# Kernel optimization log

Measured on AMD Instinct MI355X. Metric: run time of the kernel, lower is better.

The kernel has to match this reference:

```python
import jax, jax.numpy as jnp
import numpy as np

DN = ('NCHW', 'OIHW', 'NCHW')

def _conv(x, w, b, pad):
    y = jax.lax.conv_general_dilated(x, w, (1, 1), pad, dimension_numbers=DN)
    return y + b[None, :, None, None]

def setup_inputs() -> dict:
    key = jax.random.key(0)
    ks = jax.random.split(key, 8)
    B, C, H, W = 8, 256, 64, 64
    C8 = C // 8
    return {
        'x': jax.random.normal(ks[0], (B, C, H, W), jnp.float32),
        'wq': jax.random.normal(ks[1], (C8, C, 1, 3), jnp.float32) * 0.02,
        'bq': jax.random.normal(ks[2], (C8,), jnp.float32) * 0.02,
        'wk': jax.random.normal(ks[3], (C8, C, 3, 1), jnp.float32) * 0.02,
        'bk': jax.random.normal(ks[4], (C8,), jnp.float32) * 0.02,
        'wv': jax.random.normal(ks[5], (C, C, 1, 1), jnp.float32) * 0.02,
        'bv': jax.random.normal(ks[6], (C,), jnp.float32) * 0.02,
        'gamma': jax.random.normal(ks[7], (1,), jnp.float32),
    }

def reference(x, wq, bq, wk, bk, wv, bv, gamma):
    B, C, H, W = x.shape
    N = H * W
    # q: (1,3) kernel, pad (0,1); k: (3,1) kernel, pad (1,0); v: 1x1
    q = _conv(x, wq, bq, [(0, 0), (1, 1)]).reshape(B, -1, N)  # B, C/8, N
    k = _conv(x, wk, bk, [(1, 1), (0, 0)]).reshape(B, -1, N)  # B, C/8, N
    v = _conv(x, wv, bv, [(0, 0), (0, 0)]).reshape(B, C, N)   # B, C, N
    affinity = jnp.einsum('bci,bcj->bij', q, k)               # B, N, N
    affinity = jax.nn.softmax(affinity, axis=-1)
    # weights = v @ affinity^T  ->  (B, C, N)
    weights = jnp.einsum('bcj,bij->bci', v, affinity).reshape(B, C, H, W)
    return gamma[0] * weights + x
```

## Files before the change

### kernel.cpp

```cpp
#include <hip/hip_runtime.h>
#include <math.h>

#define BB 8
#define CCH 256
#define C8 32
#define NN 4096
#define LOG2E 1.44269504f

typedef unsigned short us;
typedef __attribute__((ext_vector_type(8))) short bf16x8;
typedef __attribute__((ext_vector_type(4))) float f32x4;
typedef __attribute__((ext_vector_type(16))) float f32x16;

static __device__ __forceinline__ us f2bf(float f) {
  union { float f; unsigned u; } v; v.f = f;
  unsigned r = v.u + 0x7fffu + ((v.u >> 16) & 1u);
  return (us)(r >> 16);
}
static __device__ __forceinline__ us f2bf_rhu(float f) {
  return (us)((__float_as_uint(f) + 0x8000u) >> 16);
}
template <int CTRL>
static __device__ __forceinline__ float dpp_mv(float x) {
  return __int_as_float(
      __builtin_amdgcn_update_dpp(0, __float_as_int(x), CTRL, 0xF, 0xF, false));
}
static __device__ __forceinline__ float rowsum16(float t) {
  t += dpp_mv<0x121>(t);
  t += dpp_mv<0x122>(t);
  t += dpp_mv<0x124>(t);
  t += dpp_mv<0x128>(t);
  return t;
}

__global__ __launch_bounds__(256) void prep_kernel(
    const float* __restrict__ x, const float* __restrict__ wq,
    const float* __restrict__ wk, const float* __restrict__ wv,
    us* __restrict__ xT, us* __restrict__ wqc, us* __restrict__ wkc,
    us* __restrict__ wvb) {
  __shared__ __align__(16) us lt[64 * 68];
  int bid = blockIdx.x;
  int tid = threadIdx.x;
  if (bid < 2048) {
    int b = bid >> 8, cb = (bid >> 6) & 3, nb = bid & 63;
    const float* xb = x + (((size_t)(b * 256 + cb * 64)) << 12);
    int nl = tid & 63, ch = tid >> 6;
#pragma unroll
    for (int p = 0; p < 16; p++) {
      int c = p * 4 + ch;
      lt[nl * 68 + c] = f2bf(xb[((size_t)c << 12) + (nb * 64 + nl)]);
    }
    __syncthreads();
    us* xTb = xT + (((size_t)b << 12) + nb * 64) * 256 + cb * 64;
    int cw = tid & 7, nr0 = tid >> 3;
#pragma unroll
    for (int p2 = 0; p2 < 2; p2++) {
      int nr = p2 * 32 + nr0;
      uint2 lo = *(const uint2*)&lt[nr * 68 + cw * 8];
      uint2 hi = *(const uint2*)&lt[nr * 68 + cw * 8 + 4];
      *(uint4*)&xTb[(size_t)nr * 256 + cw * 8] = make_uint4(lo.x, lo.y, hi.x, hi.y);
    }
  } else {
    int idx = (bid - 2048) * 256 + tid;
    if (idx < 24576) {
      int oc = idx / 768, r = idx % 768, t = r >> 8, ic = r & 255;
      wqc[idx] = f2bf(wq[(oc * 256 + ic) * 3 + t] * LOG2E);
    } else if (idx < 49152) {
      int j = idx - 24576;
      int oc = j / 768, r = j % 768, t = r >> 8, ic = r & 255;
      wkc[j] = f2bf(wk[(oc * 256 + ic) * 3 + t]);
    } else if (idx < 114688) {
      int j = idx - 49152;
      wvb[j] = f2bf(wv[j]);
    }
  }
}

__global__ __launch_bounds__(256) void conv_kernel(
    const us* __restrict__ xT, const us* __restrict__ wqc,
    const us* __restrict__ wkc, const float* __restrict__ bq,
    const float* __restrict__ bk, const us* __restrict__ wvb,
    const float* __restrict__ bv, us* __restrict__ qT, us* __restrict__ kT,
    us* __restrict__ vblk) {
  int tid = threadIdx.x, lane = tid & 63, w = tid >> 6;
  int l15 = lane & 15, quad = lane >> 4;
  if (blockIdx.x < 512) {
    int bid = blockIdx.x;
    int b = bid & 7, rt = bid >> 3;
    int n0 = rt * 64, y = rt;
    bool isq = (w < 2);
    int m0 = (w & 1) * 16;
    const us* wc = isq ? wqc : wkc;
    const us* xTb = xT + (((size_t)b << 12) * 256);
    f32x4 acc[4];
#pragma unroll
    for (int nt = 0; nt < 4; nt++) acc[nt] = (f32x4){0.f, 0.f, 0.f, 0.f};
#pragma unroll
    for (int t = 0; t < 3; t++) {
      bool killT = (!isq) && ((t == 0 && y == 0) || (t == 2 && y == 63));
      if (!killT) {
        int dn = isq ? (t - 1) : (t - 1) * 64;
#pragma unroll
        for (int k8 = 0; k8 < 8; k8++) {
          int kloc = t * 256 + k8 * 32 + quad * 8;
          bf16x8 af = *(const bf16x8*)(wc + (size_t)(m0 + l15) * 768 + kloc);
          int ic = k8 * 32 + quad * 8;
#pragma unroll
          for (int nt = 0; nt < 4; nt++) {
            int nl = nt * 16 + l15;
            int ns = n0 + nl + dn;
            ns = ns < 0 ? 0 : (ns > 4095 ? 4095 : ns);
            bf16x8 bf = *(const bf16x8*)(xTb + (size_t)ns * 256 + ic);
            if (isq && ((t == 0 && nl == 0) || (t == 2 && nl == 63)))
              bf = (bf16x8){0, 0, 0, 0, 0, 0, 0, 0};
            acc[nt] = __builtin_amdgcn_mfma_f32_16x16x32_bf16(af, bf, acc[nt], 0, 0, 0);
          }
        }
      }
    }
    const float* bias = isq ? bq : bk;
    float bsc = isq ? LOG2E : 1.0f;
    us* outp = (isq ? qT : kT) + (((size_t)b << 12) * 32);
    float b0 = bias[m0 + quad * 4 + 0] * bsc;
    float b1 = bias[m0 + quad * 4 + 1] * bsc;
    float b2 = bias[m0 + quad * 4 + 2] * bsc;
    float b3 = bias[m0 + quad * 4 + 3] * bsc;
#pragma unroll
    for (int nt = 0; nt < 4; nt++) {
      int n = n0 + nt * 16 + l15;
      unsigned lo = (unsigned)f2bf(acc[nt][0] + b0) | ((unsigned)f2bf(acc[nt][1] + b1) << 16);
      unsigned hi = (unsigned)f2bf(acc[nt][2] + b2) | ((unsigned)f2bf(acc[nt][3] + b3) << 16);
      *(uint2*)(outp + (size_t)n * 32 + m0 + quad * 4) = make_uint2(lo, hi);
    }
  } else {
    int bid = blockIdx.x - 512;
    int b = bid & 7, nt0 = bid >> 3;
    int n0 = nt0 * 64;
    const us* xTb = xT + (((size_t)b << 12) * 256);
    f32x4 acc[4][4];
#pragma unroll
    for (int ct = 0; ct < 4; ct++)
#pragma unroll
      for (int nt = 0; nt < 4; nt++) acc[ct][nt] = (f32x4){0.f, 0.f, 0.f, 0.f};
#pragma unroll
    for (int kk = 0; kk < 8; kk++) {
      bf16x8 bfr[4];
#pragma unroll
      for (int nt = 0; nt < 4; nt++)
        bfr[nt] = *(const bf16x8*)(xTb + (size_t)(n0 + nt * 16 + l15) * 256 + kk * 32 + quad * 8);
#pragma unroll
      for (int ct = 0; ct < 4; ct++) {
        bf16x8 af = *(const bf16x8*)(wvb + (size_t)(w * 64 + ct * 16 + l15) * 256 + kk * 32 + quad * 8);
#pragma unroll
        for (int nt = 0; nt < 4; nt++)
          acc[ct][nt] = __builtin_amdgcn_mfma_f32_16x16x32_bf16(af, bfr[nt], acc[ct][nt], 0, 0, 0);
      }
    }
    us* vb = vblk + ((size_t)b << 20);
#pragma unroll
    for (int ct = 0; ct < 4; ct++) {
#pragma unroll
      for (int r = 0; r < 4; r++) {
        int oc = w * 64 + ct * 16 + quad * 4 + r;
        float bvv = bv[oc];
#pragma unroll
        for (int nt = 0; nt < 4; nt++) {
          vb[((size_t)((n0 >> 4) + nt) * 256 + oc) * 16 + l15] = f2bf(acc[ct][nt][r] + bvv);
        }
      }
    }
  }
}

__global__ __launch_bounds__(512, 4) void attn_kernel(
    const float* __restrict__ x, const us* __restrict__ qT,
    const us* __restrict__ kT, const us* __restrict__ vblk,
    const float* __restrict__ gamma_p, float* __restrict__ out) {
  __shared__ __align__(16) us pb[2][64 * 72];
  __shared__ float lpart[2][64];

  int tid = threadIdx.x, lane = tid & 63, w = tid >> 6;
  int l15 = lane & 15, quad = lane >> 4;
  int l31 = lane & 31, h32 = lane >> 5;
  int tw = w & 3, jh = w >> 2;

  int bid = blockIdx.x;
  int b = bid & 7, i0 = (bid >> 3) * 64;

  const us* qTb = qT + (((size_t)b << 12) * 32);
  const us* kTb = kT + (((size_t)b << 12) * 32);
  const us* vbb = vblk + ((size_t)b << 20);

  bf16x8 qf = *(const bf16x8*)(qTb + (size_t)(i0 + tw * 16 + l15) * 32 + quad * 8);

  float lr[4] = {0.f, 0.f, 0.f, 0.f};
  f32x16 o[2];
#pragma unroll
  for (int it = 0; it < 2; it++)
#pragma unroll
    for (int rg = 0; rg < 16; rg++) o[it][rg] = 0.f;

  int bu = 0;
  for (int jt = 0; jt < 64; jt++) {
    int j0 = jt * 64;
    bf16x8 kf0 = *(const bf16x8*)(kTb + (size_t)(j0 + jh * 32 + l15) * 32 + quad * 8);
    bf16x8 kf1 = *(const bf16x8*)(kTb + (size_t)(j0 + jh * 32 + 16 + l15) * 32 + quad * 8);
    bf16x8 vf[4];
#pragma unroll
    for (int ks = 0; ks < 4; ks++)
      vf[ks] = *(const bf16x8*)(vbb + ((size_t)((j0 >> 4) + ks) * 256 + w * 32 + l31) * 16 + h32 * 8);
    f32x4 s0 = __builtin_amdgcn_mfma_f32_16x16x32_bf16(qf, kf0, (f32x4){0.f, 0.f, 0.f, 0.f}, 0, 0, 0);
    f32x4 s1 = __builtin_amdgcn_mfma_f32_16x16x32_bf16(qf, kf1, (f32x4){0.f, 0.f, 0.f, 0.f}, 0, 0, 0);
    us* pw = &pb[bu][(tw * 16 + quad * 4) * 72 + jh * 32 + l15];
#pragma unroll
    for (int r = 0; r < 4; r++) {
      float p0 = __builtin_amdgcn_exp2f(s0[r]);
      float p1 = __builtin_amdgcn_exp2f(s1[r]);
      lr[r] += p0 + p1;
      pw[r * 72] = f2bf_rhu(p0);
      pw[r * 72 + 16] = f2bf_rhu(p1);
    }
    __syncthreads();
#pragma unroll
    for (int ks = 0; ks < 4; ks++) {
      bf16x8 pf0 = *(const bf16x8*)&pb[bu][(size_t)l31 * 72 + ks * 16 + h32 * 8];
      bf16x8 pf1 = *(const bf16x8*)&pb[bu][(size_t)(32 + l31) * 72 + ks * 16 + h32 * 8];
      o[0] = __builtin_amdgcn_mfma_f32_32x32x16_bf16(vf[ks], pf0, o[0], 0, 0, 0);
      o[1] = __builtin_amdgcn_mfma_f32_32x32x16_bf16(vf[ks], pf1, o[1], 0, 0, 0);
    }
    bu ^= 1;
  }

  float ls[4];
#pragma unroll
  for (int r = 0; r < 4; r++) ls[r] = rowsum16(lr[r]);
  if (l15 == 0) {
#pragma unroll
    for (int r = 0; r < 4; r++) lpart[jh][tw * 16 + quad * 4 + r] = ls[r];
  }
  __syncthreads();
  float g = gamma_p[0];
  const float* xb = x + ((size_t)b << 20);
  float* ob = out + ((size_t)b << 20);
  float gl[2];
#pragma unroll
  for (int it = 0; it < 2; it++) {
    int i = it * 32 + l31;
    gl[it] = g / (lpart[0][i] + lpart[1][i]);
  }
#pragma unroll
  for (int it = 0; it < 2; it++) {
    int i = i0 + it * 32 + l31;
#pragma unroll
    for (int rg = 0; rg < 16; rg++) {
      int c = w * 32 + ((rg & 3) + 8 * (rg >> 2) + 4 * h32);
      size_t idx = ((size_t)c << 12) + i;
      ob[idx] = o[it][rg] * gl[it] + xb[idx];
    }
  }
}

extern "C" void kernel_launch(void* const* d_in, const int* in_sizes, int n_in,
                              void* d_out, int out_size, void* d_ws, size_t ws_size,
                              hipStream_t stream) {
  const float* x = (const float*)d_in[0];
  const float* wq = (const float*)d_in[1];
  const float* bq = (const float*)d_in[2];
  const float* wk = (const float*)d_in[3];
  const float* bk = (const float*)d_in[4];
  const float* wv = (const float*)d_in[5];
  const float* bv = (const float*)d_in[6];
  const float* gamma = (const float*)d_in[7];
  float* out = (float*)d_out;

  us* xT = (us*)d_ws;
  us* qT = xT + (size_t)8388608;
  us* kT = qT + (size_t)1048576;
  us* vblk = kT + (size_t)1048576;
  us* wqc = vblk + (size_t)8388608;
  us* wkc = wqc + (size_t)24576;
  us* wvb = wkc + (size_t)24576;

  prep_kernel<<<2496, 256, 0, stream>>>(x, wq, wk, wv, xT, wqc, wkc, wvb);
  conv_kernel<<<1024, 256, 0, stream>>>(xT, wqc, wkc, bq, bk, wvb, bv, qT, kT, vblk);
  attn_kernel<<<512, 512, 0, stream>>>(x, qT, kT, vblk, gamma, out);
}
```

Before: 234.0 us.

## Software-pipeline K/V loads, transpose score MFMA, pack bf16 conversions in attention loop

Restructures the attention main loop to prefetch the next tile's K and V fragments into alternate register sets, with a two-step unrolled macro. The score MFMA operands are swapped (K×Q) so each lane holds four consecutive j values, enabling packed v_cvt_pk_bf16_f32 conversions and 64-bit LDS stores of P. It adds s_setprio around the MFMA sections and an explicit lgkmcnt wait plus barrier. The row-sum reduction changes to two cross-lane shuffles. This is meant to hide global load latency and cut per-element conversion and LDS store cost, at the price of more VGPRs, which could reduce occupancy.

```diff
diff --git a/kernel.cpp b/kernel.cpp
--- a/kernel.cpp
+++ b/kernel.cpp
@@ -16,21 +16,6 @@
   union { float f; unsigned u; } v; v.f = f;
   unsigned r = v.u + 0x7fffu + ((v.u >> 16) & 1u);
   return (us)(r >> 16);
-}
-static __device__ __forceinline__ us f2bf_rhu(float f) {
-  return (us)((__float_as_uint(f) + 0x8000u) >> 16);
-}
-template <int CTRL>
-static __device__ __forceinline__ float dpp_mv(float x) {
-  return __int_as_float(
-      __builtin_amdgcn_update_dpp(0, __float_as_int(x), CTRL, 0xF, 0xF, false));
-}
-static __device__ __forceinline__ float rowsum16(float t) {
-  t += dpp_mv<0x121>(t);
-  t += dpp_mv<0x122>(t);
-  t += dpp_mv<0x124>(t);
-  t += dpp_mv<0x128>(t);
-  return t;
 }
 
 __global__ __launch_bounds__(256) void prep_kernel(
@@ -193,51 +178,100 @@
 
   bf16x8 qf = *(const bf16x8*)(qTb + (size_t)(i0 + tw * 16 + l15) * 32 + quad * 8);
 
-  float lr[4] = {0.f, 0.f, 0.f, 0.f};
-  f32x16 o[2];
-#pragma unroll
-  for (int it = 0; it < 2; it++)
-#pragma unroll
-    for (int rg = 0; rg < 16; rg++) o[it][rg] = 0.f;
-
-  int bu = 0;
-  for (int jt = 0; jt < 64; jt++) {
-    int j0 = jt * 64;
-    bf16x8 kf0 = *(const bf16x8*)(kTb + (size_t)(j0 + jh * 32 + l15) * 32 + quad * 8);
-    bf16x8 kf1 = *(const bf16x8*)(kTb + (size_t)(j0 + jh * 32 + 16 + l15) * 32 + quad * 8);
-    bf16x8 vf[4];
-#pragma unroll
-    for (int ks = 0; ks < 4; ks++)
-      vf[ks] = *(const bf16x8*)(vbb + ((size_t)((j0 >> 4) + ks) * 256 + w * 32 + l31) * 16 + h32 * 8);
-    f32x4 s0 = __builtin_amdgcn_mfma_f32_16x16x32_bf16(qf, kf0, (f32x4){0.f, 0.f, 0.f, 0.f}, 0, 0, 0);
-    f32x4 s1 = __builtin_amdgcn_mfma_f32_16x16x32_bf16(qf, kf1, (f32x4){0.f, 0.f, 0.f, 0.f}, 0, 0, 0);
-    us* pw = &pb[bu][(tw * 16 + quad * 4) * 72 + jh * 32 + l15];
-#pragma unroll
-    for (int r = 0; r < 4; r++) {
-      float p0 = __builtin_amdgcn_exp2f(s0[r]);
-      float p1 = __builtin_amdgcn_exp2f(s1[r]);
-      lr[r] += p0 + p1;
-      pw[r * 72] = f2bf_rhu(p0);
-      pw[r * 72 + 16] = f2bf_rhu(p1);
-    }
-    __syncthreads();
-#pragma unroll
-    for (int ks = 0; ks < 4; ks++) {
-      bf16x8 pf0 = *(const bf16x8*)&pb[bu][(size_t)l31 * 72 + ks * 16 + h32 * 8];
-      bf16x8 pf1 = *(const bf16x8*)&pb[bu][(size_t)(32 + l31) * 72 + ks * 16 + h32 * 8];
-      o[0] = __builtin_amdgcn_mfma_f32_32x32x16_bf16(vf[ks], pf0, o[0], 0, 0, 0);
-      o[1] = __builtin_amdgcn_mfma_f32_32x32x16_bf16(vf[ks], pf1, o[1], 0, 0, 0);
-    }
-    bu ^= 1;
-  }
-
-  float ls[4];
-#pragma unroll
-  for (int r = 0; r < 4; r++) ls[r] = rowsum16(lr[r]);
-  if (l15 == 0) {
-#pragma unroll
-    for (int r = 0; r < 4; r++) lpart[jh][tw * 16 + quad * 4 + r] = ls[r];
-  }
+  const us* kbase = kTb + (size_t)(jh * 32 + l15) * 32 + quad * 8;
+  const us* vbase = vbb + (size_t)(w * 32 + l31) * 16 + h32 * 8;
+  int pwi = (tw * 16 + l15) * 72 + jh * 32 + quad * 4;
+  int pri = l31 * 72 + h32 * 8;
+
+  float lr = 0.f;
+  f32x16 o0, o1;
+#pragma unroll
+  for (int rg = 0; rg < 16; rg++) { o0[rg] = 0.f; o1[rg] = 0.f; }
+
+  bf16x8 kA0, kA1, vA0, vA1, vA2, vA3;
+  bf16x8 kB0, kB1, vB0, vB1, vB2, vB3;
+  kA0 = *(const bf16x8*)(kbase);
+  kA1 = *(const bf16x8*)(kbase + 512);
+  vA0 = *(const bf16x8*)(vbase);
+  vA1 = *(const bf16x8*)(vbase + 4096);
+  vA2 = *(const bf16x8*)(vbase + 8192);
+  vA3 = *(const bf16x8*)(vbase + 12288);
+
+#define ATTN_STEP(JT, BUF, KC0, KC1, VC0, VC1, VC2, VC3, KN0, KN1, VN0, VN1, VN2, VN3)    \
+  {                                                                                       \
+    int jn = ((JT) + 1) & 63;                                                             \
+    const us* kp = kbase + (size_t)jn * 2048;                                             \
+    const us* vp = vbase + (size_t)jn * 16384;                                            \
+    KN0 = *(const bf16x8*)(kp);                                                           \
+    KN1 = *(const bf16x8*)(kp + 512);                                                     \
+    VN0 = *(const bf16x8*)(vp);                                                           \
+    VN1 = *(const bf16x8*)(vp + 4096);                                                    \
+    VN2 = *(const bf16x8*)(vp + 8192);                                                    \
+    VN3 = *(const bf16x8*)(vp + 12288);                                                   \
+    __builtin_amdgcn_s_setprio(1);                                                        \
+    f32x4 s0 = __builtin_amdgcn_mfma_f32_16x16x32_bf16(KC0, qf, (f32x4){0.f, 0.f, 0.f, 0.f}, 0, 0, 0); \
+    f32x4 s1 = __builtin_amdgcn_mfma_f32_16x16x32_bf16(KC1, qf, (f32x4){0.f, 0.f, 0.f, 0.f}, 0, 0, 0); \
+    __builtin_amdgcn_s_setprio(0);                                                        \
+    us* pw = (us*)pb + (BUF) * (64 * 72) + pwi;                                           \
+    {                                                                                     \
+      float p0 = __builtin_amdgcn_exp2f(s0[0]);                                           \
+      float p1 = __builtin_amdgcn_exp2f(s0[1]);                                           \
+      float p2 = __builtin_amdgcn_exp2f(s0[2]);                                           \
+      float p3 = __builtin_amdgcn_exp2f(s0[3]);                                           \
+      lr += (p0 + p1) + (p2 + p3);                                                        \
+      unsigned e0, e1;                                                                    \
+      asm("v_cvt_pk_bf16_f32 %0, %1, %2" : "=v"(e0) : "v"(p0), "v"(p1));                  \
+      asm("v_cvt_pk_bf16_f32 %0, %1, %2" : "=v"(e1) : "v"(p2), "v"(p3));                  \
+      *(uint2*)pw = make_uint2(e0, e1);                                                   \
+    }                                                                                     \
+    {                                                                                     \
+      float p0 = __builtin_amdgcn_exp2f(s1[0]);                                           \
+      float p1 = __builtin_amdgcn_exp2f(s1[1]);                                           \
+      float p2 = __builtin_amdgcn_exp2f(s1[2]);                                           \
+      float p3 = __builtin_amdgcn_exp2f(s1[3]);                                           \
+      lr += (p0 + p1) + (p2 + p3);                                                        \
+      unsigned e0, e1;                                                                    \
+      asm("v_cvt_pk_bf16_f32 %0, %1, %2" : "=v"(e0) : "v"(p0), "v"(p1));                  \
+      asm("v_cvt_pk_bf16_f32 %0, %1, %2" : "=v"(e1) : "v"(p2), "v"(p3));                  \
+      *(uint2*)(pw + 16) = make_uint2(e0, e1);                                            \
+    }                                                                                     \
+    asm volatile("s_waitcnt lgkmcnt(0)" ::: "memory");                                    \
+    __builtin_amdgcn_s_barrier();                                                         \
+    __builtin_amdgcn_sched_barrier(0);                                                    \
+    const us* pr = (const us*)pb + (BUF) * (64 * 72) + pri;                               \
+    __builtin_amdgcn_s_setprio(1);                                                        \
+    {                                                                                     \
+      bf16x8 pf0, pf1;                                                                    \
+      pf0 = *(const bf16x8*)(pr + 0);                                                     \
+      pf1 = *(const bf16x8*)(pr + 32 * 72 + 0);                                           \
+      o0 = __builtin_amdgcn_mfma_f32_32x32x16_bf16(VC0, pf0, o0, 0, 0, 0);                \
+      o1 = __builtin_amdgcn_mfma_f32_32x32x16_bf16(VC0, pf1, o1, 0, 0, 0);                \
+      pf0 = *(const bf16x8*)(pr + 16);                                                    \
+      pf1 = *(const bf16x8*)(pr + 32 * 72 + 16);                                          \
+      o0 = __builtin_amdgcn_mfma_f32_32x32x16_bf16(VC1, pf0, o0, 0, 0, 0);                \
+      o1 = __builtin_amdgcn_mfma_f32_32x32x16_bf16(VC1, pf1, o1, 0, 0, 0);                \
+      pf0 = *(const bf16x8*)(pr + 32);                                                    \
+      pf1 = *(const bf16x8*)(pr + 32 * 72 + 32);                                          \
+      o0 = __builtin_amdgcn_mfma_f32_32x32x16_bf16(VC2, pf0, o0, 0, 0, 0);                \
+      o1 = __builtin_amdgcn_mfma_f32_32x32x16_bf16(VC2, pf1, o1, 0, 0, 0);                \
+      pf0 = *(const bf16x8*)(pr + 48);                                                    \
+      pf1 = *(const bf16x8*)(pr + 32 * 72 + 48);                                          \
+      o0 = __builtin_amdgcn_mfma_f32_32x32x16_bf16(VC3, pf0, o0, 0, 0, 0);                \
+      o1 = __builtin_amdgcn_mfma_f32_32x32x16_bf16(VC3, pf1, o1, 0, 0, 0);                \
+    }                                                                                     \
+    __builtin_amdgcn_s_setprio(0);                                                        \
+  }
+
+  for (int jt2 = 0; jt2 < 32; jt2++) {
+    ATTN_STEP(2 * jt2, 0, kA0, kA1, vA0, vA1, vA2, vA3, kB0, kB1, vB0, vB1, vB2, vB3);
+    ATTN_STEP(2 * jt2 + 1, 1, kB0, kB1, vB0, vB1, vB2, vB3, kA0, kA1, vA0, vA1, vA2, vA3);
+  }
+#undef ATTN_STEP
+
+  float lt = lr;
+  lt += __shfl_xor(lt, 16);
+  lt += __shfl_xor(lt, 32);
+  if (quad == 0) lpart[jh][tw * 16 + l15] = lt;
   __syncthreads();
   float g = gamma_p[0];
   const float* xb = x + ((size_t)b << 20);
@@ -251,11 +285,12 @@
 #pragma unroll
   for (int it = 0; it < 2; it++) {
     int i = i0 + it * 32 + l31;
+    const f32x16& o = (it == 0) ? o0 : o1;
 #pragma unroll
     for (int rg = 0; rg < 16; rg++) {
       int c = w * 32 + ((rg & 3) + 8 * (rg >> 2) + 4 * h32);
       size_t idx = ((size_t)c << 12) + i;
-      ob[idx] = o[it][rg] * gl[it] + xb[idx];
+      ob[idx] = o[rg] * gl[it] + xb[idx];
     }
   }
 }
```

Result: no change. 230.5 us (-1.5%).

## Software-pipeline attention loop with register prefetch and QK/PV overlap

Applied to the files above, without the earlier changes.

Restructures the main attention loop into a manually unrolled, software-pipelined schedule. K and V tiles are prefetched two iterations ahead into rotating register sets, and the QK MFMA for the next tile is overlapped with the PV MFMAs of the previous one. It also swaps the QK operand order so each lane writes four contiguous probabilities with packed bf16 conversion (v_cvt_pk_bf16_f32) and 64-bit LDS stores. Barriers become explicit waitcnt plus s_barrier, and s_setprio is raised around the PV MFMAs. The aim is to hide global-load and LDS latency and cut the conversion and store instruction count, at the cost of higher register pressure and a more fragile schedule.

```diff
diff --git a/kernel.cpp b/kernel.cpp
--- a/kernel.cpp
+++ b/kernel.cpp
@@ -16,21 +16,6 @@
   union { float f; unsigned u; } v; v.f = f;
   unsigned r = v.u + 0x7fffu + ((v.u >> 16) & 1u);
   return (us)(r >> 16);
-}
-static __device__ __forceinline__ us f2bf_rhu(float f) {
-  return (us)((__float_as_uint(f) + 0x8000u) >> 16);
-}
-template <int CTRL>
-static __device__ __forceinline__ float dpp_mv(float x) {
-  return __int_as_float(
-      __builtin_amdgcn_update_dpp(0, __float_as_int(x), CTRL, 0xF, 0xF, false));
-}
-static __device__ __forceinline__ float rowsum16(float t) {
-  t += dpp_mv<0x121>(t);
-  t += dpp_mv<0x122>(t);
-  t += dpp_mv<0x124>(t);
-  t += dpp_mv<0x128>(t);
-  return t;
 }
 
 __global__ __launch_bounds__(256) void prep_kernel(
@@ -193,51 +178,156 @@
 
   bf16x8 qf = *(const bf16x8*)(qTb + (size_t)(i0 + tw * 16 + l15) * 32 + quad * 8);
 
-  float lr[4] = {0.f, 0.f, 0.f, 0.f};
-  f32x16 o[2];
-#pragma unroll
-  for (int it = 0; it < 2; it++)
-#pragma unroll
-    for (int rg = 0; rg < 16; rg++) o[it][rg] = 0.f;
-
-  int bu = 0;
-  for (int jt = 0; jt < 64; jt++) {
-    int j0 = jt * 64;
-    bf16x8 kf0 = *(const bf16x8*)(kTb + (size_t)(j0 + jh * 32 + l15) * 32 + quad * 8);
-    bf16x8 kf1 = *(const bf16x8*)(kTb + (size_t)(j0 + jh * 32 + 16 + l15) * 32 + quad * 8);
-    bf16x8 vf[4];
-#pragma unroll
-    for (int ks = 0; ks < 4; ks++)
-      vf[ks] = *(const bf16x8*)(vbb + ((size_t)((j0 >> 4) + ks) * 256 + w * 32 + l31) * 16 + h32 * 8);
-    f32x4 s0 = __builtin_amdgcn_mfma_f32_16x16x32_bf16(qf, kf0, (f32x4){0.f, 0.f, 0.f, 0.f}, 0, 0, 0);
-    f32x4 s1 = __builtin_amdgcn_mfma_f32_16x16x32_bf16(qf, kf1, (f32x4){0.f, 0.f, 0.f, 0.f}, 0, 0, 0);
-    us* pw = &pb[bu][(tw * 16 + quad * 4) * 72 + jh * 32 + l15];
-#pragma unroll
-    for (int r = 0; r < 4; r++) {
-      float p0 = __builtin_amdgcn_exp2f(s0[r]);
-      float p1 = __builtin_amdgcn_exp2f(s1[r]);
-      lr[r] += p0 + p1;
-      pw[r * 72] = f2bf_rhu(p0);
-      pw[r * 72 + 16] = f2bf_rhu(p1);
-    }
-    __syncthreads();
-#pragma unroll
-    for (int ks = 0; ks < 4; ks++) {
-      bf16x8 pf0 = *(const bf16x8*)&pb[bu][(size_t)l31 * 72 + ks * 16 + h32 * 8];
-      bf16x8 pf1 = *(const bf16x8*)&pb[bu][(size_t)(32 + l31) * 72 + ks * 16 + h32 * 8];
-      o[0] = __builtin_amdgcn_mfma_f32_32x32x16_bf16(vf[ks], pf0, o[0], 0, 0, 0);
-      o[1] = __builtin_amdgcn_mfma_f32_32x32x16_bf16(vf[ks], pf1, o[1], 0, 0, 0);
-    }
-    bu ^= 1;
-  }
-
-  float ls[4];
-#pragma unroll
-  for (int r = 0; r < 4; r++) ls[r] = rowsum16(lr[r]);
-  if (l15 == 0) {
-#pragma unroll
-    for (int r = 0; r < 4; r++) lpart[jh][tw * 16 + quad * 4 + r] = ls[r];
-  }
+  const us* kbase = kTb + (size_t)(jh * 32 + l15) * 32 + quad * 8;
+  const us* vbase = vbb + (size_t)(w * 32 + l31) * 16 + h32 * 8;
+  int pwi = (tw * 16 + l15) * 72 + jh * 32 + quad * 4;
+  int pri = l31 * 72 + h32 * 8;
+
+  float lr = 0.f;
+  f32x4 s0, s1;
+  f32x16 o0, o1;
+#pragma unroll
+  for (int rg = 0; rg < 16; rg++) { o0[rg] = 0.f; o1[rg] = 0.f; }
+
+  bf16x8 kS0a, kS0b, kS1a, kS1b;
+  bf16x8 v0_0, v0_1, v0_2, v0_3;
+  bf16x8 v1_0, v1_1, v1_2, v1_3;
+  bf16x8 v2_0, v2_1, v2_2, v2_3;
+  bf16x8 v3_0, v3_1, v3_2, v3_3;
+
+#define PRE(JT, KN0, KN1, VN0, VN1, VN2, VN3)                                  \
+  do {                                                                         \
+    int jn = (JT) & 63;                                                        \
+    const us* kp = kbase + (size_t)jn * 2048;                                  \
+    const us* vp = vbase + (size_t)jn * 16384;                                 \
+    KN0 = *(const bf16x8*)(kp);                                                \
+    KN1 = *(const bf16x8*)(kp + 512);                                          \
+    VN0 = *(const bf16x8*)(vp);                                                \
+    VN1 = *(const bf16x8*)(vp + 4096);                                         \
+    VN2 = *(const bf16x8*)(vp + 8192);                                         \
+    VN3 = *(const bf16x8*)(vp + 12288);                                        \
+  } while (0)
+
+#define QKM(KC0, KC1)                                                          \
+  do {                                                                         \
+    s0 = __builtin_amdgcn_mfma_f32_16x16x32_bf16(KC0, qf, (f32x4){0.f, 0.f, 0.f, 0.f}, 0, 0, 0); \
+    s1 = __builtin_amdgcn_mfma_f32_16x16x32_bf16(KC1, qf, (f32x4){0.f, 0.f, 0.f, 0.f}, 0, 0, 0); \
+  } while (0)
+
+#define PVM(BUFR, VP0, VP1, VP2, VP3)                                          \
+  do {                                                                         \
+    const us* pr = (const us*)pb + (BUFR) * (64 * 72) + pri;                   \
+    __builtin_amdgcn_s_setprio(1);                                             \
+    bf16x8 pf0, pf1;                                                           \
+    pf0 = *(const bf16x8*)(pr + 0);                                            \
+    pf1 = *(const bf16x8*)(pr + 32 * 72 + 0);                                  \
+    o0 = __builtin_amdgcn_mfma_f32_32x32x16_bf16(VP0, pf0, o0, 0, 0, 0);       \
+    o1 = __builtin_amdgcn_mfma_f32_32x32x16_bf16(VP0, pf1, o1, 0, 0, 0);       \
+    pf0 = *(const bf16x8*)(pr + 16);                                           \
+    pf1 = *(const bf16x8*)(pr + 32 * 72 + 16);                                 \
+    o0 = __builtin_amdgcn_mfma_f32_32x32x16_bf16(VP1, pf0, o0, 0, 0, 0);       \
+    o1 = __builtin_amdgcn_mfma_f32_32x32x16_bf16(VP1, pf1, o1, 0, 0, 0);       \
+    pf0 = *(const bf16x8*)(pr + 32);                                           \
+    pf1 = *(const bf16x8*)(pr + 32 * 72 + 32);                                 \
+    o0 = __builtin_amdgcn_mfma_f32_32x32x16_bf16(VP2, pf0, o0, 0, 0, 0);       \
+    o1 = __builtin_amdgcn_mfma_f32_32x32x16_bf16(VP2, pf1, o1, 0, 0, 0);       \
+    pf0 = *(const bf16x8*)(pr + 48);                                           \
+    pf1 = *(const bf16x8*)(pr + 32 * 72 + 48);                                 \
+    o0 = __builtin_amdgcn_mfma_f32_32x32x16_bf16(VP3, pf0, o0, 0, 0, 0);       \
+    o1 = __builtin_amdgcn_mfma_f32_32x32x16_bf16(VP3, pf1, o1, 0, 0, 0);       \
+    __builtin_amdgcn_s_setprio(0);                                             \
+  } while (0)
+
+#define SMW(BUFW)                                                              \
+  do {                                                                         \
+    us* pw = (us*)pb + (BUFW) * (64 * 72) + pwi;                               \
+    {                                                                          \
+      float p0 = __builtin_amdgcn_exp2f(s0[0]);                                \
+      float p1 = __builtin_amdgcn_exp2f(s0[1]);                                \
+      float p2 = __builtin_amdgcn_exp2f(s0[2]);                                \
+      float p3 = __builtin_amdgcn_exp2f(s0[3]);                                \
+      lr += (p0 + p1) + (p2 + p3);                                             \
+      unsigned e0, e1;                                                         \
+      asm("v_cvt_pk_bf16_f32 %0, %1, %2" : "=v"(e0) : "v"(p0), "v"(p1));       \
+      asm("v_cvt_pk_bf16_f32 %0, %1, %2" : "=v"(e1) : "v"(p2), "v"(p3));       \
+      *(uint2*)pw = make_uint2(e0, e1);                                        \
+    }                                                                          \
+    {                                                                          \
+      float p0 = __builtin_amdgcn_exp2f(s1[0]);                                \
+      float p1 = __builtin_amdgcn_exp2f(s1[1]);                                \
+      float p2 = __builtin_amdgcn_exp2f(s1[2]);                                \
+      float p3 = __builtin_amdgcn_exp2f(s1[3]);                                \
+      lr += (p0 + p1) + (p2 + p3);                                             \
+      unsigned e0, e1;                                                         \
+      asm("v_cvt_pk_bf16_f32 %0, %1, %2" : "=v"(e0) : "v"(p0), "v"(p1));       \
+      asm("v_cvt_pk_bf16_f32 %0, %1, %2" : "=v"(e1) : "v"(p2), "v"(p3));       \
+      *(uint2*)(pw + 16) = make_uint2(e0, e1);                                 \
+    }                                                                          \
+  } while (0)
+
+#define BAR                                                                    \
+  do {                                                                         \
+    asm volatile("s_waitcnt lgkmcnt(0)" ::: "memory");                         \
+    __builtin_amdgcn_s_barrier();                                              \
+    __builtin_amdgcn_sched_barrier(0);                                         \
+  } while (0)
+
+  PRE(0, kS0a, kS0b, v0_0, v0_1, v0_2, v0_3);
+  PRE(1, kS1a, kS1b, v1_0, v1_1, v1_2, v1_3);
+  QKM(kS0a, kS0b);
+  SMW(0);
+  BAR;
+  PRE(2, kS0a, kS0b, v2_0, v2_1, v2_2, v2_3);
+  QKM(kS1a, kS1b);
+  PVM(0, v0_0, v0_1, v0_2, v0_3);
+  SMW(1);
+  BAR;
+  PRE(3, kS1a, kS1b, v3_0, v3_1, v3_2, v3_3);
+  QKM(kS0a, kS0b);
+  PVM(1, v1_0, v1_1, v1_2, v1_3);
+  SMW(0);
+  BAR;
+  PRE(4, kS0a, kS0b, v0_0, v0_1, v0_2, v0_3);
+  QKM(kS1a, kS1b);
+  PVM(0, v2_0, v2_1, v2_2, v2_3);
+  SMW(1);
+  BAR;
+
+  for (int n4 = 1; n4 < 16; n4++) {
+    int n = n4 * 4;
+    PRE(n + 1, kS1a, kS1b, v1_0, v1_1, v1_2, v1_3);
+    QKM(kS0a, kS0b);
+    PVM(1, v3_0, v3_1, v3_2, v3_3);
+    SMW(0);
+    BAR;
+    PRE(n + 2, kS0a, kS0b, v2_0, v2_1, v2_2, v2_3);
+    QKM(kS1a, kS1b);
+    PVM(0, v0_0, v0_1, v0_2, v0_3);
+    SMW(1);
+    BAR;
+    PRE(n + 3, kS1a, kS1b, v3_0, v3_1, v3_2, v3_3);
+    QKM(kS0a, kS0b);
+    PVM(1, v1_0, v1_1, v1_2, v1_3);
+    SMW(0);
+    BAR;
+    PRE(n + 4, kS0a, kS0b, v0_0, v0_1, v0_2, v0_3);
+    QKM(kS1a, kS1b);
+    PVM(0, v2_0, v2_1, v2_2, v2_3);
+    SMW(1);
+    BAR;
+  }
+  PVM(1, v3_0, v3_1, v3_2, v3_3);
+
+#undef PRE
+#undef QKM
+#undef PVM
+#undef SMW
+#undef BAR
+
+  float lt = lr;
+  lt += __shfl_xor(lt, 16);
+  lt += __shfl_xor(lt, 32);
+  if (quad == 0) lpart[jh][tw * 16 + l15] = lt;
   __syncthreads();
   float g = gamma_p[0];
   const float* xb = x + ((size_t)b << 20);
@@ -251,11 +341,12 @@
 #pragma unroll
   for (int it = 0; it < 2; it++) {
     int i = i0 + it * 32 + l31;
+    const f32x16& o = (it == 0) ? o0 : o1;
 #pragma unroll
     for (int rg = 0; rg < 16; rg++) {
       int c = w * 32 + ((rg & 3) + 8 * (rg >> 2) + 4 * h32);
       size_t idx = ((size_t)c << 12) + i;
-      ob[idx] = o[it][rg] * gl[it] + xb[idx];
+      ob[idx] = o[rg] * gl[it] + xb[idx];
     }
   }
 }
```

After: 228.1 us. 1.03x faster.

## Widen attention key tile to 128 and software-pipeline K/V prefetch

Applied to the files above, without the earlier changes.

The attention loop now processes 128 keys per step instead of 64, which halves the number of block barriers. It prefetches the next K tile into alternating register sets while the current tile is consumed. QK MFMA operands are swapped so each lane holds contiguous probabilities, which are packed to bf16 with v_cvt_pk_bf16_f32 and written as 8-byte LDS stores. MFMA sections are raised with s_setprio and the barrier is hand-written. The cost is higher register and LDS usage, which may lower occupancy under launch_bounds(512,4).

```diff
diff --git a/kernel.cpp b/kernel.cpp
--- a/kernel.cpp
+++ b/kernel.cpp
@@ -1,10 +1,6 @@
 #include <hip/hip_runtime.h>
 #include <math.h>
 
-#define BB 8
-#define CCH 256
-#define C8 32
-#define NN 4096
 #define LOG2E 1.44269504f
 
 typedef unsigned short us;
@@ -16,21 +12,6 @@
   union { float f; unsigned u; } v; v.f = f;
   unsigned r = v.u + 0x7fffu + ((v.u >> 16) & 1u);
   return (us)(r >> 16);
-}
-static __device__ __forceinline__ us f2bf_rhu(float f) {
-  return (us)((__float_as_uint(f) + 0x8000u) >> 16);
-}
-template <int CTRL>
-static __device__ __forceinline__ float dpp_mv(float x) {
-  return __int_as_float(
-      __builtin_amdgcn_update_dpp(0, __float_as_int(x), CTRL, 0xF, 0xF, false));
-}
-static __device__ __forceinline__ float rowsum16(float t) {
-  t += dpp_mv<0x121>(t);
-  t += dpp_mv<0x122>(t);
-  t += dpp_mv<0x124>(t);
-  t += dpp_mv<0x128>(t);
-  return t;
 }
 
 __global__ __launch_bounds__(256) void prep_kernel(
@@ -176,7 +157,7 @@
     const float* __restrict__ x, const us* __restrict__ qT,
     const us* __restrict__ kT, const us* __restrict__ vblk,
     const float* __restrict__ gamma_p, float* __restrict__ out) {
-  __shared__ __align__(16) us pb[2][64 * 72];
+  __shared__ __align__(16) us pb[2][64 * 136];
   __shared__ float lpart[2][64];
 
   int tid = threadIdx.x, lane = tid & 63, w = tid >> 6;
@@ -193,51 +174,134 @@
 
   bf16x8 qf = *(const bf16x8*)(qTb + (size_t)(i0 + tw * 16 + l15) * 32 + quad * 8);
 
-  float lr[4] = {0.f, 0.f, 0.f, 0.f};
-  f32x16 o[2];
-#pragma unroll
-  for (int it = 0; it < 2; it++)
-#pragma unroll
-    for (int rg = 0; rg < 16; rg++) o[it][rg] = 0.f;
-
-  int bu = 0;
-  for (int jt = 0; jt < 64; jt++) {
-    int j0 = jt * 64;
-    bf16x8 kf0 = *(const bf16x8*)(kTb + (size_t)(j0 + jh * 32 + l15) * 32 + quad * 8);
-    bf16x8 kf1 = *(const bf16x8*)(kTb + (size_t)(j0 + jh * 32 + 16 + l15) * 32 + quad * 8);
-    bf16x8 vf[4];
-#pragma unroll
-    for (int ks = 0; ks < 4; ks++)
-      vf[ks] = *(const bf16x8*)(vbb + ((size_t)((j0 >> 4) + ks) * 256 + w * 32 + l31) * 16 + h32 * 8);
-    f32x4 s0 = __builtin_amdgcn_mfma_f32_16x16x32_bf16(qf, kf0, (f32x4){0.f, 0.f, 0.f, 0.f}, 0, 0, 0);
-    f32x4 s1 = __builtin_amdgcn_mfma_f32_16x16x32_bf16(qf, kf1, (f32x4){0.f, 0.f, 0.f, 0.f}, 0, 0, 0);
-    us* pw = &pb[bu][(tw * 16 + quad * 4) * 72 + jh * 32 + l15];
-#pragma unroll
-    for (int r = 0; r < 4; r++) {
-      float p0 = __builtin_amdgcn_exp2f(s0[r]);
-      float p1 = __builtin_amdgcn_exp2f(s1[r]);
-      lr[r] += p0 + p1;
-      pw[r * 72] = f2bf_rhu(p0);
-      pw[r * 72 + 16] = f2bf_rhu(p1);
-    }
-    __syncthreads();
-#pragma unroll
-    for (int ks = 0; ks < 4; ks++) {
-      bf16x8 pf0 = *(const bf16x8*)&pb[bu][(size_t)l31 * 72 + ks * 16 + h32 * 8];
-      bf16x8 pf1 = *(const bf16x8*)&pb[bu][(size_t)(32 + l31) * 72 + ks * 16 + h32 * 8];
-      o[0] = __builtin_amdgcn_mfma_f32_32x32x16_bf16(vf[ks], pf0, o[0], 0, 0, 0);
-      o[1] = __builtin_amdgcn_mfma_f32_32x32x16_bf16(vf[ks], pf1, o[1], 0, 0, 0);
-    }
-    bu ^= 1;
-  }
-
-  float ls[4];
-#pragma unroll
-  for (int r = 0; r < 4; r++) ls[r] = rowsum16(lr[r]);
-  if (l15 == 0) {
-#pragma unroll
-    for (int r = 0; r < 4; r++) lpart[jh][tw * 16 + quad * 4 + r] = ls[r];
-  }
+  const us* kbase = kTb + (size_t)(jh * 64 + l15) * 32 + quad * 8;
+  const us* vbase = vbb + (size_t)(w * 32 + l31) * 16 + h32 * 8;
+  int pwi = (tw * 16 + l15) * 136 + jh * 64 + quad * 4;
+  int pri = l31 * 136 + h32 * 8;
+
+  float lr = 0.f;
+  f32x4 s0, s1, s2, s3;
+  f32x16 o0, o1;
+#pragma unroll
+  for (int rg = 0; rg < 16; rg++) { o0[rg] = 0.f; o1[rg] = 0.f; }
+
+  bf16x8 kX0, kX1, kX2, kX3, kY0, kY1, kY2, kY3;
+  bf16x8 vf0, vf1, vf2, vf3, vf4, vf5, vf6, vf7;
+
+#define PREK(N, K0, K1, K2, K3)                                                \
+  do {                                                                         \
+    const us* kp = kbase + (size_t)((N) & 31) * 4096;                          \
+    K0 = *(const bf16x8*)(kp);                                                 \
+    K1 = *(const bf16x8*)(kp + 512);                                           \
+    K2 = *(const bf16x8*)(kp + 1024);                                          \
+    K3 = *(const bf16x8*)(kp + 1536);                                          \
+  } while (0)
+
+#define PREV(N)                                                                \
+  do {                                                                         \
+    const us* vp = vbase + (size_t)((N) & 31) * 32768;                         \
+    vf0 = *(const bf16x8*)(vp);                                                \
+    vf1 = *(const bf16x8*)(vp + 4096);                                         \
+    vf2 = *(const bf16x8*)(vp + 8192);                                         \
+    vf3 = *(const bf16x8*)(vp + 12288);                                        \
+    vf4 = *(const bf16x8*)(vp + 16384);                                        \
+    vf5 = *(const bf16x8*)(vp + 20480);                                        \
+    vf6 = *(const bf16x8*)(vp + 24576);                                        \
+    vf7 = *(const bf16x8*)(vp + 28672);                                        \
+  } while (0)
+
+#define QKM(K0, K1, K2, K3)                                                    \
+  do {                                                                         \
+    __builtin_amdgcn_s_setprio(1);                                             \
+    s0 = __builtin_amdgcn_mfma_f32_16x16x32_bf16(K0, qf, (f32x4){0.f, 0.f, 0.f, 0.f}, 0, 0, 0); \
+    s1 = __builtin_amdgcn_mfma_f32_16x16x32_bf16(K1, qf, (f32x4){0.f, 0.f, 0.f, 0.f}, 0, 0, 0); \
+    s2 = __builtin_amdgcn_mfma_f32_16x16x32_bf16(K2, qf, (f32x4){0.f, 0.f, 0.f, 0.f}, 0, 0, 0); \
+    s3 = __builtin_amdgcn_mfma_f32_16x16x32_bf16(K3, qf, (f32x4){0.f, 0.f, 0.f, 0.f}, 0, 0, 0); \
+    __builtin_amdgcn_s_setprio(0);                                             \
+  } while (0)
+
+#define SMW1(SR, PWOFF)                                                        \
+  do {                                                                         \
+    float p0 = __builtin_amdgcn_exp2f(SR[0]);                                  \
+    float p1 = __builtin_amdgcn_exp2f(SR[1]);                                  \
+    float p2 = __builtin_amdgcn_exp2f(SR[2]);                                  \
+    float p3 = __builtin_amdgcn_exp2f(SR[3]);                                  \
+    lr += (p0 + p1) + (p2 + p3);                                               \
+    unsigned e0, e1;                                                           \
+    asm("v_cvt_pk_bf16_f32 %0, %1, %2" : "=v"(e0) : "v"(p0), "v"(p1));         \
+    asm("v_cvt_pk_bf16_f32 %0, %1, %2" : "=v"(e1) : "v"(p2), "v"(p3));         \
+    *(uint2*)(pw + (PWOFF)) = make_uint2(e0, e1);                              \
+  } while (0)
+
+#define SMW(BUF)                                                               \
+  do {                                                                         \
+    us* pw = (us*)pb + (BUF) * (64 * 136) + pwi;                               \
+    SMW1(s0, 0);                                                               \
+    SMW1(s1, 16);                                                              \
+    SMW1(s2, 32);                                                              \
+    SMW1(s3, 48);                                                              \
+  } while (0)
+
+#define BAR                                                                    \
+  do {                                                                         \
+    asm volatile("s_waitcnt lgkmcnt(0)" ::: "memory");                         \
+    __builtin_amdgcn_s_barrier();                                              \
+    __builtin_amdgcn_sched_barrier(0);                                         \
+  } while (0)
+
+#define PV1(VF, KSOFF)                                                         \
+  do {                                                                         \
+    bf16x8 pf0 = *(const bf16x8*)(pr + (KSOFF));                               \
+    bf16x8 pf1 = *(const bf16x8*)(pr + 32 * 136 + (KSOFF));                    \
+    o0 = __builtin_amdgcn_mfma_f32_32x32x16_bf16(VF, pf0, o0, 0, 0, 0);        \
+    o1 = __builtin_amdgcn_mfma_f32_32x32x16_bf16(VF, pf1, o1, 0, 0, 0);        \
+  } while (0)
+
+#define PVM(BUF)                                                               \
+  do {                                                                         \
+    const us* pr = (const us*)pb + (BUF) * (64 * 136) + pri;                   \
+    __builtin_amdgcn_s_setprio(1);                                             \
+    PV1(vf0, 0);                                                               \
+    PV1(vf1, 16);                                                              \
+    PV1(vf2, 32);                                                              \
+    PV1(vf3, 48);                                                              \
+    PV1(vf4, 64);                                                              \
+    PV1(vf5, 80);                                                              \
+    PV1(vf6, 96);                                                              \
+    PV1(vf7, 112);                                                             \
+    __builtin_amdgcn_s_setprio(0);                                             \
+  } while (0)
+
+  PREK(0, kX0, kX1, kX2, kX3);
+  for (int n2 = 0; n2 < 16; n2++) {
+    int n = n2 * 2;
+    QKM(kX0, kX1, kX2, kX3);
+    PREV(n);
+    PREK(n + 1, kY0, kY1, kY2, kY3);
+    SMW(0);
+    BAR;
+    PVM(0);
+    QKM(kY0, kY1, kY2, kY3);
+    PREV(n + 1);
+    PREK(n + 2, kX0, kX1, kX2, kX3);
+    SMW(1);
+    BAR;
+    PVM(1);
+  }
+
+#undef PREK
+#undef PREV
+#undef QKM
+#undef SMW1
+#undef SMW
+#undef BAR
+#undef PV1
+#undef PVM
+
+  float lt = lr;
+  lt += __shfl_xor(lt, 16);
+  lt += __shfl_xor(lt, 32);
+  if (quad == 0) lpart[jh][tw * 16 + l15] = lt;
   __syncthreads();
   float g = gamma_p[0];
   const float* xb = x + ((size_t)b << 20);
@@ -251,11 +315,12 @@
 #pragma unroll
   for (int it = 0; it < 2; it++) {
     int i = i0 + it * 32 + l31;
+    const f32x16& o = (it == 0) ? o0 : o1;
 #pragma unroll
     for (int rg = 0; rg < 16; rg++) {
       int c = w * 32 + ((rg & 3) + 8 * (rg >> 2) + 4 * h32);
       size_t idx = ((size_t)c << 12) + i;
-      ob[idx] = o[it][rg] * gl[it] + xb[idx];
+      ob[idx] = o[rg] * gl[it] + xb[idx];
     }
   }
 }
```

Result: no change. 231.2 us (-1.2%).
